# Optimization experiments

Hardware: AMD Instinct MI355X
Metric: run time of the kernel (lower is better)

## Reference

```python
import jax, jax.numpy as jnp
import numpy as np

NSAMPLE = 64
RADIUS = 0.3
HMIN = -0.2
HMAX_LIST = (0.1, 0.2, 0.3, 0.4)
NUM_ANGLE = 12
NUM_DEPTH = 4
EPS = 1e-5


def setup_inputs() -> dict:
    key = jax.random.key(0)
    ks = jax.random.split(key, 32)
    rn = lambda i, s: jax.random.normal(ks[i], s, dtype=jnp.float32)
    ru = lambda i, s: jax.random.uniform(ks[i], s, dtype=jnp.float32)
    return {
        'seed_xyz': rn(0, (2, 1024, 3)),
        'pointcloud': rn(1, (2, 8192, 3)),
        'vp_rot': rn(2, (2, 1024, 3, 3)),
        'cw1': rn(3, (64, 3)), 'cbn1': ru(4, (4, 64)),
        'cw2': rn(5, (128, 64)), 'cbn2': ru(6, (4, 128)),
        'cw3': rn(7, (256, 128)), 'cbn3': ru(8, (4, 256)),
        'ow1': rn(9, (128, 256)), 'ob1': rn(10, (128,)), 'obn1': ru(11, (4, 128)),
        'ow2': rn(12, (128, 128)), 'ob2': rn(13, (128,)), 'obn2': ru(14, (4, 128)),
        'ow3': rn(15, (36, 128)), 'ob3': rn(16, (36,)),
        'tw1': rn(17, (128, 256)), 'tb1': rn(18, (128,)), 'tbn1': ru(19, (4, 128)),
        'tw2': rn(20, (128, 128)), 'tb2': rn(21, (128,)), 'tbn2': ru(22, (4, 128)),
        'tw3': rn(23, (12, 128)), 'tb3': rn(24, (12,)),
    }


def _bn_relu(y, bn):
    g, b, m, v = bn[0], bn[1], bn[2], bn[3]
    return jax.nn.relu(g * (y - m) * jax.lax.rsqrt(v + EPS) + b)


def _bn(y, bn):
    g, b, m, v = bn[0], bn[1], bn[2], bn[3]
    return g * (y - m) * jax.lax.rsqrt(v + EPS) + b


def _forward(seed_xyz, pointcloud, vp_rot, cw1, cbn1, cw2, cbn2, cw3, cbn3,
             ow1, ob1, obn1, ow2, ob2, obn2, ow3, ob3,
             tw1, tb1, tbn1, tw2, tb2, tbn2, tw3, tb3):
    B, ns, _ = seed_xyz.shape
    N = pointcloud.shape[1]
    # relative coords of every scene point w.r.t. every seed, rotated into the
    # grasp-view frame (cylinder axis = x after rotation): (B, ns, N, 3)
    rel = pointcloud[:, None, :, :] - seed_xyz[:, :, None, :]
    rot_rel = jnp.einsum('bsnc,bscd->bsnd', rel, vp_rot)
    ax = rot_rel[..., 0]
    r2 = rot_rel[..., 1] ** 2 + rot_rel[..., 2] ** 2
    pref = jnp.arange(N, dtype=jnp.float32) / N  # earlier index preferred (CUDA scan order)
    groups = []
    for hmax in HMAX_LIST:
        mask = (ax > HMIN) & (ax < hmax) & (r2 < RADIUS * RADIUS)
        score = mask.astype(jnp.float32) * 2.0 - pref
        _, idx = jax.lax.top_k(score, NSAMPLE)  # (B, ns, NSAMPLE), first valid idxs in order
        valid = jnp.take_along_axis(mask, idx, axis=-1)
        idx = jnp.where(valid, idx, idx[..., :1])  # fill slots with first found index
        g = jnp.take_along_axis(rot_rel, idx[..., None], axis=2)  # (B, ns, NSAMPLE, 3)
        groups.append(g)
    feat = jnp.stack(groups, axis=2)  # (B, ns, num_depth, NSAMPLE, 3)
    feat = feat.reshape(B, ns * NUM_DEPTH, NSAMPLE, 3)
    # SharedMLP [3,64,128,256], conv2d 1x1 (no bias) + BN + ReLU
    h = _bn_relu(feat @ cw1.T, cbn1)
    h = _bn_relu(h @ cw2.T, cbn2)
    h = _bn_relu(h @ cw3.T, cbn3)
    vp = jnp.max(h, axis=2)  # max-pool over nsample -> (B, ns*num_depth, 256)

    def head(w1, b1, bn1, w2, b2, bn2, w3, b3):
        x = _bn_relu(vp @ w1.T + b1, bn1)
        x = _bn_relu(x @ w2.T + b2, bn2)
        return x @ w3.T + b3

    op = head(ow1, ob1, obn1, ow2, ob2, obn2, ow3, ob3)     # (B, ns*D, 3*num_angle)
    tol = head(tw1, tb1, tbn1, tw2, tb2, tbn2, tw3, tb3)    # (B, ns*D, num_angle)
    out = jnp.concatenate([op, tol], axis=-1)               # score|angle_cls|width|tolerance
    out = out.reshape(B, ns, NUM_DEPTH, 4 * NUM_ANGLE).transpose(0, 3, 1, 2)
    return out  # (B, 4*num_angle, num_seed, num_depth)


def reference(seed_xyz, pointcloud, vp_rot, cw1, cbn1, cw2, cbn2, cw3, cbn3,
              ow1, ob1, obn1, ow2, ob2, obn2, ow3, ob3,
              tw1, tb1, tbn1, tw2, tb2, tbn2, tw3, tb3):
    return _forward(seed_xyz, pointcloud, vp_rot, cw1, cbn1, cw2, cbn2, cw3, cbn3,
                    ow1, ob1, obn1, ow2, ob2, obn2, ow3, ob3,
                    tw1, tb1, tbn1, tw2, tb2, tbn2, tw3, tb3)
```

## Files before the change

kernel.cpp:

```cpp
#include <hip/hip_runtime.h>
#include <hip/hip_bf16.h>

#define NB    2
#define NS    1024
#define NPTS  8192
#define NGROUP (NB*NS*4)

enum : int {
  OFF_BW2  = 256,
  OFF_W1Q  = 4352,
  OFF_B2   = 8448,
  OFF_BW3  = 8576,
  OFF_B3   = 41344,
  OFF_HB1  = 41600,
  OFF_HB1B = 74368,
  OFF_HB2  = 74624,
  OFF_HB2B = 107392,
  OFF_HB3  = 107648,
  OFF_HB3B = 115840,
  OFF_PCX  = 1719552, OFF_PCY = 1735936, OFF_PCZ = 1752320,
  OFF_SEED = 1768704, OFF_ROT = 1774848,
  OFF_FLAG = 3824896,
  PREP_TOTAL = 189632 + 6144 + 18432 + 49152,
};

struct Ptrs { const void* p[25]; };

typedef __attribute__((ext_vector_type(8))) short bf16x8;
typedef __attribute__((ext_vector_type(4))) float f32x4;
typedef __attribute__((ext_vector_type(4))) unsigned u32x4;

template<typename T> struct LD;
template<> struct LD<float> {
  static __device__ __forceinline__ float get(const void* p, int i){ return ((const float*)p)[i]; }
};
template<> struct LD<__hip_bfloat16> {
  static __device__ __forceinline__ float get(const void* p, int i){ return __bfloat162float(((const __hip_bfloat16*)p)[i]); }
};

template<typename T>
__device__ __forceinline__ float bnscale(const void* bn, int C, int c){
  float g = LD<T>::get(bn, c);
  float v = LD<T>::get(bn, 3*C + c);
  return g / sqrtf(v + 1e-5f);
}

__device__ __forceinline__ unsigned short f2bf(float v){
  __hip_bfloat16 hb = __float2bfloat16(v);
  return *reinterpret_cast<unsigned short*>(&hb);
}

#if __has_builtin(__builtin_amdgcn_cvt_pk_bf16_f32)
typedef __attribute__((ext_vector_type(2))) __bf16 bf16x2_t;
__device__ __forceinline__ unsigned pk2bf(float a, float b){
  bf16x2_t r = __builtin_amdgcn_cvt_pk_bf16_f32(a, b);
  return *reinterpret_cast<unsigned*>(&r);
}
#else
__device__ __forceinline__ unsigned pk2bf(float a, float b){
  return (unsigned)f2bf(a) | ((unsigned)f2bf(b) << 16);
}
#endif

template<typename T>
__device__ void prep_body(const Ptrs& in, float* __restrict__ ws, int i){
  if (i < 256) { int c = i>>2, d = i&3; float s = bnscale<T>(in.p[4],64,c);
    float v = (d<3) ? LD<T>::get(in.p[3], c*3+d)*s
                    : LD<T>::get(in.p[4],64+c) - LD<T>::get(in.p[4],2*64+c)*s;
    ws[OFF_W1Q+i] = v; return; }
  i -= 256;
  if (i < 8192) {
    int j = i&7, f = i>>3, lane = f&63, kn = f>>6, kt = kn&1, nt = kn>>1;
    int n = nt*16 + (lane&15), k = kt*32 + ((lane>>4)<<3) + j;
    float s = bnscale<T>(in.p[6],128,n);
    ((unsigned short*)(ws + OFF_BW2))[i] = f2bf(LD<T>::get(in.p[5], n*64+k)*s); return; }
  i -= 8192;
  if (i < 32768) {
    int j = i&7, f = i>>3, lane = f&63, kn = f>>6, kt = kn&3, nt = kn>>2;
    int n = nt*16 + (lane&15), k = kt*32 + ((lane>>4)<<3) + j;
    float s = bnscale<T>(in.p[8],256,n);
    ((unsigned short*)(ws + OFF_BW3))[i] = f2bf(LD<T>::get(in.p[7], n*128+k)*s); return; }
  i -= 32768;
  if (i < 128) { float s = bnscale<T>(in.p[6],128,i);
    ws[OFF_B2+i] = LD<T>::get(in.p[6],128+i) - LD<T>::get(in.p[6],2*128+i)*s; return; }
  i -= 128;
  if (i < 256) { float s = bnscale<T>(in.p[8],256,i);
    ws[OFF_B3+i] = LD<T>::get(in.p[8],256+i) - LD<T>::get(in.p[8],2*256+i)*s; return; }
  i -= 256;
  if (i < 65536) {
    int j = i&7, f = i>>3, lane = f&63, kn = f>>6, kt = kn&7, nt = kn>>3;
    int n = nt*16 + (lane&15), k = kt*32 + ((lane>>4)<<3) + j;
    float v;
    if (n < 128) v = LD<T>::get(in.p[9],  n*256+k)       * bnscale<T>(in.p[11],128,n);
    else         v = LD<T>::get(in.p[17], (n-128)*256+k) * bnscale<T>(in.p[19],128,n-128);
    ((unsigned short*)(ws + OFF_HB1))[i] = f2bf(v); return; }
  i -= 65536;
  if (i < 256) { int n = i; float v;
    if (n < 128) { float s = bnscale<T>(in.p[11],128,n);
      v = (LD<T>::get(in.p[10],n) - LD<T>::get(in.p[11],2*128+n))*s + LD<T>::get(in.p[11],128+n); }
    else { int m = n-128; float s = bnscale<T>(in.p[19],128,m);
      v = (LD<T>::get(in.p[18],m) - LD<T>::get(in.p[19],2*128+m))*s + LD<T>::get(in.p[19],128+m); }
    ws[OFF_HB1B+n] = v; return; }
  i -= 256;
  if (i < 65536) {
    int j = i&7, f = i>>3, lane = f&63, kn = f>>6, kt = kn&7, nt = kn>>3;
    int n = nt*16 + (lane&15), k = kt*32 + ((lane>>4)<<3) + j;
    float v = 0.f;
    if (n < 128) { if (k < 128)  v = LD<T>::get(in.p[12], n*128+k)            * bnscale<T>(in.p[14],128,n); }
    else         { if (k >= 128) v = LD<T>::get(in.p[20], (n-128)*128+(k-128)) * bnscale<T>(in.p[22],128,n-128); }
    ((unsigned short*)(ws + OFF_HB2))[i] = f2bf(v); return; }
  i -= 65536;
  if (i < 256) { int n = i; float v;
    if (n < 128) { float s = bnscale<T>(in.p[14],128,n);
      v = (LD<T>::get(in.p[13],n) - LD<T>::get(in.p[14],2*128+n))*s + LD<T>::get(in.p[14],128+n); }
    else { int m = n-128; float s = bnscale<T>(in.p[22],128,m);
      v = (LD<T>::get(in.p[21],m) - LD<T>::get(in.p[22],2*128+m))*s + LD<T>::get(in.p[22],128+m); }
    ws[OFF_HB2B+n] = v; return; }
  i -= 256;
  if (i < 16384) {
    int j = i&7, f = i>>3, lane = f&63, kn = f>>6, kt = kn&7, nt = kn>>3;
    int n = nt*16 + (lane&15), k = kt*32 + ((lane>>4)<<3) + j;
    float v = 0.f;
    if (n < 36)      { if (k < 128)  v = LD<T>::get(in.p[15], n*128+k); }
    else if (n < 48) { if (k >= 128) v = LD<T>::get(in.p[23], (n-36)*128+(k-128)); }
    ((unsigned short*)(ws + OFF_HB3))[i] = f2bf(v); return; }
  i -= 16384;
  if (i < 64) { int n = i; float v = 0.f;
    if (n < 36) v = LD<T>::get(in.p[16], n);
    else if (n < 48) v = LD<T>::get(in.p[24], n-36);
    ws[OFF_HB3B+n] = v; return; }
  i -= 64;
  if (i < 6144)  { ws[OFF_SEED+i] = LD<T>::get(in.p[0], i); return; }
  i -= 6144;
  if (i < 18432) { ws[OFF_ROT+i] = LD<T>::get(in.p[2], i); return; }
  i -= 18432;
  { int arr = i >> 14, idx = i & 16383;
    ws[OFF_PCX + arr*16384 + idx] = LD<T>::get(in.p[1], idx*3 + arr); }
}

__global__ __launch_bounds__(256) void prep_kernel(Ptrs in, float* __restrict__ ws){
  __shared__ int sf;
  const int t = threadIdx.x;
  if (t == 0) sf = 0;
  __syncthreads();
  int loc = 0;
  const uint4* w3r = (const uint4*)in.p[7];
#pragma unroll
  for (int k = 0; k < 2; ++k) {
    uint4 u = w3r[t + k*256];
    loc |= ((u.x & 0x7F80u) == 0x7F80u) | (((u.x>>16) & 0x7F80u) == 0x7F80u);
    loc |= ((u.y & 0x7F80u) == 0x7F80u) | (((u.y>>16) & 0x7F80u) == 0x7F80u);
    loc |= ((u.z & 0x7F80u) == 0x7F80u) | (((u.z>>16) & 0x7F80u) == 0x7F80u);
    loc |= ((u.w & 0x7F80u) == 0x7F80u) | (((u.w>>16) & 0x7F80u) == 0x7F80u);
  }
  if (loc) atomicOr(&sf, 1);
  __syncthreads();
  const int isf32 = sf;
  const int i = blockIdx.x*256 + t;
  if (i == 0) ((int*)(ws + OFF_FLAG))[0] = isf32;
  if (i >= PREP_TOTAL) return;
  if (isf32) prep_body<float>(in, ws, i);
  else       prep_body<__hip_bfloat16>(in, ws, i);
}

__device__ void group_phase(const float* __restrict__ ws, float* __restrict__ scratch,
                            int* __restrict__ cl, float* __restrict__ p0s,
                            float* __restrict__ featL, int* __restrict__ mtL,
                            int blk, int t){
#pragma clang fp contract(off)
  const int wave = t >> 6, lane = t & 63;
  const int s = wave >> 1, half = wave & 1;
  const int seedIdx = blk*2 + s;
  const int b = seedIdx >> 10;
  const float sx = ws[OFF_SEED + seedIdx*3+0];
  const float sy = ws[OFF_SEED + seedIdx*3+1];
  const float sz = ws[OFF_SEED + seedIdx*3+2];
  const float r00=ws[OFF_ROT+seedIdx*9+0], r01=ws[OFF_ROT+seedIdx*9+1], r02=ws[OFF_ROT+seedIdx*9+2];
  const float r10=ws[OFF_ROT+seedIdx*9+3], r11=ws[OFF_ROT+seedIdx*9+4], r12=ws[OFF_ROT+seedIdx*9+5];
  const float r20=ws[OFF_ROT+seedIdx*9+6], r21=ws[OFF_ROT+seedIdx*9+7], r22=ws[OFF_ROT+seedIdx*9+8];
  const float* px = ws + OFF_PCX + b*8192;
  const float* py = ws + OFF_PCY + b*8192;
  const float* pz = ws + OFF_PCZ + b*8192;
  if (half == 0 && lane == 0) {
    float e0 = px[0] - sx, e1 = py[0] - sy, e2 = pz[0] - sz;
    p0s[s*3+0] = e0*r00 + e1*r10 + e2*r20;
    p0s[s*3+1] = e0*r01 + e1*r11 + e2*r21;
    p0s[s*3+2] = e0*r02 + e1*r12 + e2*r22;
  }
  float* s0 = scratch + ((s*2+half)*4+0)*192;
  float* s1 = scratch + ((s*2+half)*4+1)*192;
  float* s2 = scratch + ((s*2+half)*4+2)*192;
  float* s3 = scratch + ((s*2+half)*4+3)*192;
  int c0n=0, c1n=0, c2n=0, c3n=0;
  const int basept = half*4096;
  const unsigned long long pm = (1ull << lane) - 1ull;

  auto scan = [&](float x, float y, float z){
    float e0 = x - sx, e1 = y - sy, e2 = z - sz;
    float rx = e0*r00 + e1*r10 + e2*r20;
    float ry = e0*r01 + e1*r11 + e2*r21;
    float rz = e0*r02 + e1*r12 + e2*r22;
    float r2 = ry*ry + rz*rz;
    const bool mb = (rx > -0.2f) && (r2 < 0.09f);
    const bool l3 = mb && (rx < 0.4f);
    const unsigned long long bal3 = __ballot(l3);
    if (bal3 == 0ull) return;
    { bool m = mb && (rx < 0.1f); unsigned long long bal = __ballot(m);
      if (bal) { int slot = c0n + __popcll(bal & pm);
        if (m && slot < 64) { s0[slot*3]=rx; s0[slot*3+1]=ry; s0[slot*3+2]=rz; }
        c0n += __popcll(bal); } }
    { bool m = mb && (rx < 0.2f); unsigned long long bal = __ballot(m);
      if (bal) { int slot = c1n + __popcll(bal & pm);
        if (m && slot < 64) { s1[slot*3]=rx; s1[slot*3+1]=ry; s1[slot*3+2]=rz; }
        c1n += __popcll(bal); } }
    { bool m = mb && (rx < 0.3f); unsigned long long bal = __ballot(m);
      if (bal) { int slot = c2n + __popcll(bal & pm);
        if (m && slot < 64) { s2[slot*3]=rx; s2[slot*3+1]=ry; s2[slot*3+2]=rz; }
        c2n += __popcll(bal); } }
    { int slot = c3n + __popcll(bal3 & pm);
      if (l3 && slot < 64) { s3[slot*3]=rx; s3[slot*3+1]=ry; s3[slot*3+2]=rz; }
      c3n += __popcll(bal3); }
  };

  for (int c = 0; c < 64; c += 2) {
    const int i0 = basept + c*64 + lane;
    float xA = px[i0],    yA = py[i0],    zA = pz[i0];
    float xB = px[i0+64], yB = py[i0+64], zB = pz[i0+64];
    scan(xA, yA, zA);
    scan(xB, yB, zB);
  }
  if (lane == 0) {
    cl[(s*2+half)*4+0]=c0n; cl[(s*2+half)*4+1]=c1n;
    cl[(s*2+half)*4+2]=c2n; cl[(s*2+half)*4+3]=c3n;
  }
  __syncthreads();
  for (int idx = t; idx < 512; idx += 256) {
    const int ss = idx >> 8, bin = (idx >> 6) & 3, slot = idx & 63;
    int ca = cl[(ss*2+0)*4+bin]; if (ca > 64) ca = 64;
    int cb = cl[(ss*2+1)*4+bin];
    const float* A = scratch + ((ss*2+0)*4+bin)*192;
    const float* B = scratch + ((ss*2+1)*4+bin)*192;
    float fx, fy, fz;
    if (slot < ca)              { fx=A[slot*3]; fy=A[slot*3+1]; fz=A[slot*3+2]; }
    else if (slot - ca < cb)    { int q = slot-ca; fx=B[q*3]; fy=B[q*3+1]; fz=B[q*3+2]; }
    else if (ca > 0)            { fx=A[0]; fy=A[1]; fz=A[2]; }
    else if (cb > 0)            { fx=B[0]; fy=B[1]; fz=B[2]; }
    else                        { fx=p0s[ss*3+0]; fy=p0s[ss*3+1]; fz=p0s[ss*3+2]; }
    float* fo = featL + (ss*4+bin)*192;
    fo[slot*3+0]=fx; fo[slot*3+1]=fy; fo[slot*3+2]=fz;
  }
  if (t < 8) {
    const int ss = t >> 2, bin = t & 3;
    int tot = cl[(ss*2+0)*4+bin] + cl[(ss*2+1)*4+bin];
    if (tot > 64) tot = 64;
    if (tot < 1)  tot = 1;
    mtL[t] = (tot + 15) >> 4;
  }
}

template<int MTS>
__device__ __forceinline__ void mlp_body(const float* __restrict__ ws, unsigned short* __restrict__ h2,
                                         const float* __restrict__ wq, const float* __restrict__ featp,
                                         float* __restrict__ vpp,
                                         int lane, int quad, int l15, int nhalf){
  float fx[MTS], fy[MTS], fz[MTS];
#pragma unroll
  for (int Nt = 0; Nt < MTS; ++Nt) {
    const int sm = Nt*16 + l15;
    fx[Nt] = featp[sm*3+0]; fy[Nt] = featp[sm*3+1]; fz[Nt] = featp[sm*3+2];
  }
  bf16x8 b1[MTS][2];
#pragma unroll
  for (int kt = 0; kt < 2; ++kt) {
    f32x4 w[8];
#pragma unroll
    for (int j = 0; j < 8; ++j) w[j] = *(const f32x4*)(wq + (kt*32 + quad*8 + j)*4);
#pragma unroll
    for (int Nt = 0; Nt < MTS; ++Nt) {
      const float x0 = fx[Nt], x1 = fy[Nt], x2 = fz[Nt];
      u32x4 p;
#pragma unroll
      for (int jp = 0; jp < 4; ++jp) {
        const f32x4 wa = w[2*jp], wb = w[2*jp+1];
        const float v0 = fmaxf(wa[3] + x0*wa[0] + x1*wa[1] + x2*wa[2], 0.f);
        const float v1 = fmaxf(wb[3] + x0*wb[0] + x1*wb[1] + x2*wb[2], 0.f);
        p[jp] = pk2bf(v0, v1);
      }
      b1[Nt][kt] = __builtin_bit_cast(bf16x8, p);
    }
  }
  const bf16x8* BW2 = (const bf16x8*)(ws + OFF_BW2);
#pragma unroll
  for (int mt4 = 0; mt4 < 4; ++mt4) {
    const int Mt = nhalf*4 + mt4;
    const f32x4 bias4 = *(const f32x4*)(ws + OFF_B2 + Mt*16 + quad*4);
    f32x4 acc[MTS];
#pragma unroll
    for (int Nt = 0; Nt < MTS; ++Nt) acc[Nt] = bias4;
#pragma unroll
    for (int kt = 0; kt < 2; ++kt) {
      const bf16x8 aw = BW2[(Mt*2+kt)*64 + lane];
#pragma unroll
      for (int Nt = 0; Nt < MTS; ++Nt)
        acc[Nt] = __builtin_amdgcn_mfma_f32_16x16x32_bf16(aw, b1[Nt][kt], acc[Nt], 0, 0, 0);
    }
#pragma unroll
    for (int Nt = 0; Nt < MTS; ++Nt) {
      const unsigned lo = pk2bf(fmaxf(acc[Nt][0],0.f), fmaxf(acc[Nt][1],0.f));
      const unsigned hi = pk2bf(fmaxf(acc[Nt][2],0.f), fmaxf(acc[Nt][3],0.f));
      uint2* dst = (uint2*)&h2[(Nt*16 + l15)*136 + Mt*16 + quad*4];
      *dst = make_uint2(lo, hi);
    }
  }
  __syncthreads();
  bf16x8 a2[MTS][4];
#pragma unroll
  for (int mt = 0; mt < MTS; ++mt)
#pragma unroll
    for (int kt = 0; kt < 4; ++kt)
      a2[mt][kt] = *(const bf16x8*)&h2[(mt*16 + l15)*136 + kt*32 + quad*8];
  const bf16x8* BW3 = (const bf16x8*)(ws + OFF_BW3);
  float vpv[8];
#pragma unroll
  for (int nt8 = 0; nt8 < 8; ++nt8) {
    const int nt = nhalf*8 + nt8;
    const int n = nt*16 + l15;
    const float bias = ws[OFF_B3 + n];
    f32x4 acc[MTS];
#pragma unroll
    for (int mt = 0; mt < MTS; ++mt) acc[mt] = (f32x4){bias, bias, bias, bias};
#pragma unroll
    for (int kt = 0; kt < 4; ++kt) {
      const bf16x8 b = BW3[(nt*4+kt)*64 + lane];
#pragma unroll
      for (int mt = 0; mt < MTS; ++mt)
        acc[mt] = __builtin_amdgcn_mfma_f32_16x16x32_bf16(a2[mt][kt], b, acc[mt], 0, 0, 0);
    }
    float mx = 0.f;
#pragma unroll
    for (int mt = 0; mt < MTS; ++mt)
      mx = fmaxf(mx, fmaxf(fmaxf(acc[mt][0], acc[mt][1]), fmaxf(acc[mt][2], acc[mt][3])));
    mx = fmaxf(mx, __shfl_xor(mx, 16, 64));
    mx = fmaxf(mx, __shfl_xor(mx, 32, 64));
    vpv[nt8] = mx;
  }
  if (quad == 0) {
#pragma unroll
    for (int nt8 = 0; nt8 < 8; ++nt8) vpp[nhalf*128 + nt8*16 + l15] = vpv[nt8];
  }
}

#define YSTRIDE 264
__global__ __launch_bounds__(256) void fused_kernel(float* __restrict__ ws, void* __restrict__ outv){
  __shared__ __align__(16) char ubuf[34816];
  __shared__ float featL[8*192];
  __shared__ float vpL[8*256];
  __shared__ int   mtL[8];
  __shared__ float w1qL[1024];
  const int t = threadIdx.x;
  const int wave = t >> 6, lane = t & 63;
  const int quad = lane >> 4, l15 = lane & 15;
  const int blk = blockIdx.x;

  for (int i = t; i < 1024; i += 256) w1qL[i] = ws[OFF_W1Q + i];

  group_phase(ws, (float*)ubuf, (int*)(ubuf + 12288), (float*)(ubuf + 12288 + 64),
              featL, mtL, blk, t);
  __syncthreads();

  {
    const int grp = wave >> 1, nhalf = wave & 1;
    unsigned short* h2 = (unsigned short*)ubuf + grp*(64*136);
    for (int pair = 0; pair < 4; ++pair) {
      const int m0 = mtL[pair*2], m1 = mtL[pair*2+1];
      const int v = (m0 > m1) ? m0 : m1;
      const int lg = pair*2 + grp;
      const float* featp = featL + lg*192;
      float* vpp = vpL + lg*256;
      switch (v) {
        case 1:  mlp_body<1>(ws, h2, w1qL, featp, vpp, lane, quad, l15, nhalf); break;
        case 2:  mlp_body<2>(ws, h2, w1qL, featp, vpp, lane, quad, l15, nhalf); break;
        case 3:  mlp_body<3>(ws, h2, w1qL, featp, vpp, lane, quad, l15, nhalf); break;
        default: mlp_body<4>(ws, h2, w1qL, featp, vpp, lane, quad, l15, nhalf); break;
      }
      __syncthreads();
    }
  }

  {
    const int isf32 = ((const volatile int*)(ws + OFF_FLAG))[0];
    unsigned short* y = (unsigned short*)ubuf;
    bf16x8 a[8];
    if (l15 < 8) {
      const float* vp = vpL + l15*256;
#pragma unroll
      for (int kt = 0; kt < 8; ++kt) {
        const float4* v4 = (const float4*)(vp + kt*32 + quad*8);
        float4 u0 = v4[0], u1 = v4[1];
        a[kt][0]=(short)f2bf(u0.x); a[kt][1]=(short)f2bf(u0.y); a[kt][2]=(short)f2bf(u0.z); a[kt][3]=(short)f2bf(u0.w);
        a[kt][4]=(short)f2bf(u1.x); a[kt][5]=(short)f2bf(u1.y); a[kt][6]=(short)f2bf(u1.z); a[kt][7]=(short)f2bf(u1.w);
      }
    } else {
      const u32x4 z = (u32x4){0,0,0,0};
#pragma unroll
      for (int kt = 0; kt < 8; ++kt) a[kt] = __builtin_bit_cast(bf16x8, z);
    }
    const bf16x8* HB1 = (const bf16x8*)(ws + OFF_HB1);
#pragma unroll
    for (int nt4 = 0; nt4 < 4; ++nt4) {
      const int nt = wave*4 + nt4;
      const int n = nt*16 + l15;
      const float bias = ws[OFF_HB1B + n];
      f32x4 acc = (f32x4){bias, bias, bias, bias};
#pragma unroll
      for (int kt = 0; kt < 8; ++kt)
        acc = __builtin_amdgcn_mfma_f32_16x16x32_bf16(a[kt], HB1[(nt*8+kt)*64 + lane], acc, 0, 0, 0);
#pragma unroll
      for (int jj = 0; jj < 4; ++jj)
        y[(quad*4+jj)*YSTRIDE + n] = f2bf(fmaxf(acc[jj], 0.f));
    }
    __syncthreads();
#pragma unroll
    for (int kt = 0; kt < 8; ++kt)
      a[kt] = *(const bf16x8*)&y[l15*YSTRIDE + kt*32 + quad*8];
    __syncthreads();
    const bf16x8* HB2 = (const bf16x8*)(ws + OFF_HB2);
#pragma unroll
    for (int nt4 = 0; nt4 < 4; ++nt4) {
      const int nt = wave*4 + nt4;
      const int n = nt*16 + l15;
      const float bias = ws[OFF_HB2B + n];
      f32x4 acc = (f32x4){bias, bias, bias, bias};
#pragma unroll
      for (int kt = 0; kt < 8; ++kt)
        acc = __builtin_amdgcn_mfma_f32_16x16x32_bf16(a[kt], HB2[(nt*8+kt)*64 + lane], acc, 0, 0, 0);
#pragma unroll
      for (int jj = 0; jj < 4; ++jj)
        y[(quad*4+jj)*YSTRIDE + n] = f2bf(fmaxf(acc[jj], 0.f));
    }
    __syncthreads();
#pragma unroll
    for (int kt = 0; kt < 8; ++kt)
      a[kt] = *(const bf16x8*)&y[l15*YSTRIDE + kt*32 + quad*8];
    const bf16x8* HB3 = (const bf16x8*)(ws + OFF_HB3);
    {
      const int n = wave*16 + l15;
      const float bias = ws[OFF_HB3B + n];
      f32x4 acc = (f32x4){bias, bias, bias, bias};
#pragma unroll
      for (int kt = 0; kt < 8; ++kt)
        acc = __builtin_amdgcn_mfma_f32_16x16x32_bf16(a[kt], HB3[(wave*8+kt)*64 + lane], acc, 0, 0, 0);
      if (n < 48 && quad < 2) {
#pragma unroll
        for (int jj = 0; jj < 4; ++jj) {
          const int gr = blk*8 + quad*4 + jj;
          const int b = gr >> 12, rem = gr & 4095, s = rem >> 2, d = rem & 3;
          const int o = ((b*48 + n)*1024 + s)*4 + d;
          if (isf32) ((float*)outv)[o] = acc[jj];
          else       ((__hip_bfloat16*)outv)[o] = __float2bfloat16(acc[jj]);
        }
      }
    }
  }
}

extern "C" void kernel_launch(void* const* d_in, const int* in_sizes, int n_in,
                              void* d_out, int out_size, void* d_ws, size_t ws_size,
                              hipStream_t stream) {
  float* ws = (float*)d_ws;
  Ptrs P;
  for (int i = 0; i < 25; ++i) P.p[i] = d_in[i];
  prep_kernel<<<(PREP_TOTAL+255)/256, 256, 0, stream>>>(P, ws);
  fused_kernel<<<NB*NS/2, 256, 0, stream>>>(ws, d_out);
}
```

Measured before the change: 208.0 us.

## Split each group's MLP across all four waves and halve LDS footprint

```diff
diff --git a/kernel.cpp b/kernel.cpp
--- a/kernel.cpp
+++ b/kernel.cpp
@@ -262,7 +262,7 @@
 __device__ __forceinline__ void mlp_body(const float* __restrict__ ws, unsigned short* __restrict__ h2,
                                          const float* __restrict__ wq, const float* __restrict__ featp,
                                          float* __restrict__ vpp,
-                                         int lane, int quad, int l15, int nhalf){
+                                         int lane, int quad, int l15, int wave){
   float fx[MTS], fy[MTS], fz[MTS];
 #pragma unroll
   for (int Nt = 0; Nt < MTS; ++Nt) {
@@ -291,8 +291,8 @@
   }
   const bf16x8* BW2 = (const bf16x8*)(ws + OFF_BW2);
 #pragma unroll
-  for (int mt4 = 0; mt4 < 4; ++mt4) {
-    const int Mt = nhalf*4 + mt4;
+  for (int mt2 = 0; mt2 < 2; ++mt2) {
+    const int Mt = wave*2 + mt2;
     const f32x4 bias4 = *(const f32x4*)(ws + OFF_B2 + Mt*16 + quad*4);
     f32x4 acc[MTS];
 #pragma unroll
@@ -320,10 +320,9 @@
     for (int kt = 0; kt < 4; ++kt)
       a2[mt][kt] = *(const bf16x8*)&h2[(mt*16 + l15)*136 + kt*32 + quad*8];
   const bf16x8* BW3 = (const bf16x8*)(ws + OFF_BW3);
-  float vpv[8];
-#pragma unroll
-  for (int nt8 = 0; nt8 < 8; ++nt8) {
-    const int nt = nhalf*8 + nt8;
+#pragma unroll
+  for (int nt4 = 0; nt4 < 4; ++nt4) {
+    const int nt = wave*4 + nt4;
     const int n = nt*16 + l15;
     const float bias = ws[OFF_B3 + n];
     f32x4 acc[MTS];
@@ -342,17 +341,13 @@
       mx = fmaxf(mx, fmaxf(fmaxf(acc[mt][0], acc[mt][1]), fmaxf(acc[mt][2], acc[mt][3])));
     mx = fmaxf(mx, __shfl_xor(mx, 16, 64));
     mx = fmaxf(mx, __shfl_xor(mx, 32, 64));
-    vpv[nt8] = mx;
-  }
-  if (quad == 0) {
-#pragma unroll
-    for (int nt8 = 0; nt8 < 8; ++nt8) vpp[nhalf*128 + nt8*16 + l15] = vpv[nt8];
+    if (quad == 0) vpp[nt*16 + l15] = mx;
   }
 }
 
 #define YSTRIDE 264
-__global__ __launch_bounds__(256) void fused_kernel(float* __restrict__ ws, void* __restrict__ outv){
-  __shared__ __align__(16) char ubuf[34816];
+__global__ __launch_bounds__(256, 4) void fused_kernel(float* __restrict__ ws, void* __restrict__ outv){
+  __shared__ __align__(16) char ubuf[17408];
   __shared__ float featL[8*192];
   __shared__ float vpL[8*256];
   __shared__ int   mtL[8];
@@ -361,6 +356,7 @@
   const int wave = t >> 6, lane = t & 63;
   const int quad = lane >> 4, l15 = lane & 15;
   const int blk = blockIdx.x;
+  const int isf32 = ((const volatile int*)(ws + OFF_FLAG))[0];
 
   for (int i = t; i < 1024; i += 256) w1qL[i] = ws[OFF_W1Q + i];
 
@@ -369,26 +365,22 @@
   __syncthreads();
 
   {
-    const int grp = wave >> 1, nhalf = wave & 1;
-    unsigned short* h2 = (unsigned short*)ubuf + grp*(64*136);
-    for (int pair = 0; pair < 4; ++pair) {
-      const int m0 = mtL[pair*2], m1 = mtL[pair*2+1];
-      const int v = (m0 > m1) ? m0 : m1;
-      const int lg = pair*2 + grp;
-      const float* featp = featL + lg*192;
-      float* vpp = vpL + lg*256;
+    unsigned short* h2 = (unsigned short*)ubuf;
+    for (int gi = 0; gi < 8; ++gi) {
+      const int v = mtL[gi];
+      const float* featp = featL + gi*192;
+      float* vpp = vpL + gi*256;
       switch (v) {
-        case 1:  mlp_body<1>(ws, h2, w1qL, featp, vpp, lane, quad, l15, nhalf); break;
-        case 2:  mlp_body<2>(ws, h2, w1qL, featp, vpp, lane, quad, l15, nhalf); break;
-        case 3:  mlp_body<3>(ws, h2, w1qL, featp, vpp, lane, quad, l15, nhalf); break;
-        default: mlp_body<4>(ws, h2, w1qL, featp, vpp, lane, quad, l15, nhalf); break;
+        case 1:  mlp_body<1>(ws, h2, w1qL, featp, vpp, lane, quad, l15, wave); break;
+        case 2:  mlp_body<2>(ws, h2, w1qL, featp, vpp, lane, quad, l15, wave); break;
+        case 3:  mlp_body<3>(ws, h2, w1qL, featp, vpp, lane, quad, l15, wave); break;
+        default: mlp_body<4>(ws, h2, w1qL, featp, vpp, lane, quad, l15, wave); break;
       }
       __syncthreads();
     }
   }
 
   {
-    const int isf32 = ((const volatile int*)(ws + OFF_FLAG))[0];
     unsigned short* y = (unsigned short*)ubuf;
     bf16x8 a[8];
     if (l15 < 8) {
```

Result: no change. 212.0 us (+1.9%).
